# Performance work log

Hardware: AMD Instinct MI355X
Metric: run time of the kernel (lower is better)

The kernel has to match this reference:

```python
import math
import jax, jax.numpy as jnp
import numpy as np

B, C, N, T = 16, 64, 1024, 12


def setup_inputs() -> dict:
    key = jax.random.key(0)
    ks = jax.random.split(key, 12)
    s = 1.0 / math.sqrt(C)
    inp = {
        "input": jax.random.normal(ks[0], (B, C, N, T), dtype=jnp.float32),
        # 1x1 conv weights stored as [out_c, in_c] (squeeze of [C,C,1,1])
        "qw": jax.random.normal(ks[1], (C, C), dtype=jnp.float32) * s,
        "qb": jnp.zeros((C,), dtype=jnp.float32),
        "vw": jax.random.normal(ks[2], (C, C), dtype=jnp.float32) * s,
        "vb": jnp.zeros((C,), dtype=jnp.float32),
        "cw": jax.random.normal(ks[3], (C, C), dtype=jnp.float32) * s,
        "cb": jnp.zeros((C,), dtype=jnp.float32),
        # memory: xavier_uniform over (C, N)
        "memory": jax.random.uniform(ks[4], (C, N), dtype=jnp.float32,
                                      minval=-1.0, maxval=1.0) * math.sqrt(6.0 / (C + N)),
        # fc: Linear(2,8) -> ReLU -> Linear(8,1); torch Linear weight is [out,in]
        "fc1w": jax.random.normal(ks[5], (8, 2), dtype=jnp.float32) * (1.0 / math.sqrt(2.0)),
        "fc1b": jnp.zeros((8,), dtype=jnp.float32),
        "fc2w": jax.random.normal(ks[6], (1, 8), dtype=jnp.float32) * (1.0 / math.sqrt(8.0)),
        "fc2b": jnp.zeros((1,), dtype=jnp.float32),
    }
    return inp


def _conv1x1(x, w, b):
    # Conv2d(C,C,(1,1)) + ReLU (dropout is identity in eval)
    return jax.nn.relu(jnp.einsum('oc,bcnt->bont', w, x) + b[None, :, None, None])


def reference(input, qw, qb, vw, vb, cw, cb, memory, fc1w, fc1b, fc2w, fc2b):
    query = _conv1x1(input, qw, qb)           # [B,C,N,T]
    value = _conv1x1(input, vw, vb)           # [B,C,N,T]
    c = query.shape[1]
    inv_sqrt_c = 1.0 / math.sqrt(c)

    # dynamic adjacency 1: query x memory
    a1 = jax.nn.softmax(
        jax.nn.relu(jnp.einsum('bcnt,cm->bnm', query, memory) * inv_sqrt_c), axis=-1)
    # dynamic adjacency 2: time-pooled query self-similarity
    qs = query.sum(-1)                        # [B,C,N]
    a2 = jax.nn.softmax(
        jax.nn.relu(jnp.einsum('bcn,bcm->bnm', qs, qs) * inv_sqrt_c), axis=-1)

    adj_f = jnp.stack([a1, a2], axis=-1)      # [B,N,N,2]
    h = jax.nn.relu(adj_f @ fc1w.T + fc1b)    # [B,N,N,8]
    adj_f = jax.nn.softmax((h @ fc2w.T + fc2b)[..., 0], axis=-1)  # [B,N,N]

    # top-k mask (k = 0.8*N), scatter 1s at topk indices
    k = int(adj_f.shape[1] * 0.8)
    _, topk_idx = jax.lax.top_k(adj_f, k)     # [B,N,k]
    bsz, n, _ = adj_f.shape
    bi = jnp.arange(bsz)[:, None, None]
    ni = jnp.arange(n)[None, :, None]
    mask = jnp.zeros_like(adj_f).at[bi, ni, topk_idx].set(1.0)
    adj_f = adj_f * mask

    # aggregation: bmm over flattened (C*T)
    b_, cc, nn_, t = value.shape
    vr = value.transpose(0, 2, 1, 3).reshape(b_, nn_, cc * t)   # [B,N,C*T]
    agg = adj_f @ vr                                            # [B,N,C*T]
    agg = agg.reshape(b_, nn_, cc, t).transpose(0, 2, 1, 3)     # [B,C,N,T]

    return _conv1x1(agg, cw, cb)
```

## Files before the change

### kernel.cpp

```cpp
#include <hip/hip_runtime.h>

using u32 = unsigned int;
using u64 = unsigned long long;
using u16 = unsigned short;

typedef __attribute__((ext_vector_type(8))) short bf16x8;
typedef __attribute__((ext_vector_type(4))) float f32x4;

__device__ __forceinline__ u16 f2bf(float f) {
  u32 u = __float_as_uint(f);
  u += 0x7FFFu + ((u >> 16) & 1u);
  return (u16)(u >> 16);
}

__device__ __forceinline__ float wredMaxF(float v) {
#pragma unroll
  for (int o = 32; o > 0; o >>= 1) v = fmaxf(v, __shfl_xor(v, o, 64));
  return v;
}
__device__ __forceinline__ double wredSumD(double v) {
#pragma unroll
  for (int o = 32; o > 0; o >>= 1) v += __shfl_xor(v, o, 64);
  return v;
}

__device__ __forceinline__ float fexpf64(double x) {
  const double INVLN2 = 1.4426950408889634074;
  const double NLN2HI = -6.93147180369123816490e-01;
  const double NLN2LO = -1.90821492927058770002e-10;
  double kd = rint(x * INVLN2);
  double r = fma(kd, NLN2HI, x);
  r = fma(kd, NLN2LO, r);
  double p = 2.08767569878680990e-09;
  p = fma(p, r, 2.50521083854417188e-08);
  p = fma(p, r, 2.75573192239858907e-07);
  p = fma(p, r, 2.75573192239858925e-06);
  p = fma(p, r, 2.48015873015873016e-05);
  p = fma(p, r, 1.98412698412698413e-04);
  p = fma(p, r, 1.38888888888888889e-03);
  p = fma(p, r, 8.33333333333333333e-03);
  p = fma(p, r, 4.16666666666666667e-02);
  p = fma(p, r, 1.66666666666666667e-01);
  p = fma(p, r, 5.0e-01);
  p = fma(p, r, 1.0);
  p = fma(p, r, 1.0);
  int k = (int)kd;
  if (k < -1022) k = -1022;
  double s = __hiloint2double((1023 + k) << 20, 0);
  return (float)(p * s);
}

__global__ __launch_bounds__(512) void k_conv_q(
    const float* __restrict__ x, const float* __restrict__ qw, const float* __restrict__ qb,
    double* __restrict__ qs64, float* __restrict__ qs32T)
{
  __shared__ __align__(16) double Xs64[8 * 384];
  __shared__ float wqT[64 * 65];
  __shared__ float qbL[64];
  const int tid = threadIdx.x;
  const int b = blockIdx.y;
  const int n0 = blockIdx.x * 8;

#pragma unroll
  for (int j = 0; j < 8; ++j) {
    int idx = tid + 512 * j;
    int o = idx >> 6, c = idx & 63;
    wqT[c * 65 + o] = qw[idx];
  }
  if (tid < 64) qbL[tid] = qb[tid];

  const int co = tid & 63;
  const int r = tid >> 6;
  double q0[12];
#pragma unroll
  for (int t = 0; t < 12; ++t) q0[t] = 0.0;

  for (int p = 0; p < 2; ++p) {
    __syncthreads();
#pragma unroll
    for (int j = 0; j < 3; ++j) {
      int d2 = tid + 512 * j;
      int d = d2 * 2;
      int rr = d / 384;
      int rem = d - rr * 384;
      int cl = rem / 12;
      int t = rem - cl * 12;
      float2 f = *(const float2*)&x[(((size_t)(b * 64 + p * 32 + cl)) * 1024 + n0 + rr) * 12 + t];
      double2 dv;
      dv.x = (double)f.x;
      dv.y = (double)f.y;
      *(double2*)&Xs64[d] = dv;
    }
    __syncthreads();

    const double* xrow = &Xs64[r * 384];
#pragma unroll 2
    for (int cl = 0; cl < 32; ++cl) {
      double wd = (double)wqT[(p * 32 + cl) * 65 + co];
      double xd[12];
#pragma unroll
      for (int k = 0; k < 6; ++k)
        *(double2*)&xd[2 * k] = *(const double2*)&xrow[cl * 12 + 2 * k];
#pragma unroll
      for (int t = 0; t < 12; ++t) q0[t] = fma(wd, xd[t], q0[t]);
    }
  }

  const float qbv = qbL[co];
  double sA = 0.0;
#pragma unroll
  for (int t = 0; t < 12; ++t) {
    float qa = fmaxf((float)q0[t] + qbv, 0.f);
    sA += (double)qa;
  }
  qs64[((size_t)(b * 1024 + n0 + r)) * 64 + co] = sA;
  qs32T[((size_t)(b * 64 + co)) * 1024 + n0 + r] = (float)sA;
}

__global__ __launch_bounds__(256) void k_conv_v(
    const float* __restrict__ x, const float* __restrict__ vw, const float* __restrict__ vb,
    u16* __restrict__ vr)
{
  __shared__ float Xs[8 * 768];
  __shared__ float wvT[64 * 64];
  const int tid = threadIdx.x;
  const int b = blockIdx.y;
  const int n0 = blockIdx.x * 8;

#pragma unroll
  for (int j = 0; j < 4; ++j) {
    int lin = (tid + 256 * j) * 4;
    int c = lin >> 6, o0 = lin & 63;
    float4 wv4;
    wv4.x = vw[(o0 + 0) * 64 + c];
    wv4.y = vw[(o0 + 1) * 64 + c];
    wv4.z = vw[(o0 + 2) * 64 + c];
    wv4.w = vw[(o0 + 3) * 64 + c];
    *(float4*)&wvT[lin] = wv4;
  }
#pragma unroll
  for (int j = 0; j < 6; ++j) {
    int q = tid + 256 * j;
    int pr = q / 3, s = q - pr * 3;
    int c = pr >> 3, nl = pr & 7;
    *(float4*)&Xs[nl * 768 + c * 12 + s * 4] =
        *(const float4*)&x[(((size_t)(b * 64 + c)) * 1024 + n0 + nl) * 12 + s * 4];
  }
  __syncthreads();

  const int co = tid & 63;
  const int nlA = tid >> 6;
  const int nlB = nlA + 4;
  float v0[12], v1[12];
#pragma unroll
  for (int t = 0; t < 12; ++t) { v0[t] = 0.f; v1[t] = 0.f; }

  for (int c = 0; c < 64; ++c) {
    float wvv = wvT[c * 64 + co];
    float xA[12], xB[12];
    *(float4*)&xA[0] = *(float4*)&Xs[nlA * 768 + c * 12 + 0];
    *(float4*)&xA[4] = *(float4*)&Xs[nlA * 768 + c * 12 + 4];
    *(float4*)&xA[8] = *(float4*)&Xs[nlA * 768 + c * 12 + 8];
    *(float4*)&xB[0] = *(float4*)&Xs[nlB * 768 + c * 12 + 0];
    *(float4*)&xB[4] = *(float4*)&Xs[nlB * 768 + c * 12 + 4];
    *(float4*)&xB[8] = *(float4*)&Xs[nlB * 768 + c * 12 + 8];
#pragma unroll
    for (int t = 0; t < 12; ++t) {
      v0[t] += wvv * xA[t];
      v1[t] += wvv * xB[t];
    }
  }

  const float vbv = vb[co];
  size_t vb0 = ((size_t)(b * 1024 + n0 + nlA)) * 768 + co * 12;
  size_t vb1 = ((size_t)(b * 1024 + n0 + nlB)) * 768 + co * 12;
#pragma unroll
  for (int i = 0; i < 6; ++i) {
    u32 p0 = (u32)f2bf(fmaxf(v0[2 * i] + vbv, 0.f)) | ((u32)f2bf(fmaxf(v0[2 * i + 1] + vbv, 0.f)) << 16);
    *(u32*)&vr[vb0 + 2 * i] = p0;
    u32 p1 = (u32)f2bf(fmaxf(v1[2 * i] + vbv, 0.f)) | ((u32)f2bf(fmaxf(v1[2 * i + 1] + vbv, 0.f)) << 16);
    *(u32*)&vr[vb1 + 2 * i] = p1;
  }
}

__global__ __launch_bounds__(256) void k_transpose_vr(const u16* __restrict__ vr, u16* __restrict__ vrT)
{
  __shared__ u16 Tt[64 * 72];
  const int tid = threadIdx.x;
  const int b = blockIdx.z;
  const int ct0 = blockIdx.x * 64;
  const int m0 = blockIdx.y * 64;
#pragma unroll
  for (int j = 0; j < 2; ++j) {
    int idx = tid + 256 * j;
    int r = idx >> 3, s = idx & 7;
    u16 tmp[8];
    *(uint4*)tmp = *(const uint4*)&vr[((size_t)(b * 1024 + m0 + r)) * 768 + ct0 + s * 8];
#pragma unroll
    for (int jj = 0; jj < 8; ++jj) Tt[(s * 8 + jj) * 72 + r] = tmp[jj];
  }
  __syncthreads();
#pragma unroll
  for (int j = 0; j < 2; ++j) {
    int idx = tid + 256 * j;
    int r2 = idx >> 3, s2 = idx & 7;
    *(uint4*)&vrT[((size_t)(b * 768 + ct0 + r2)) * 1024 + m0 + s2 * 8] =
        *(const uint4*)&Tt[r2 * 72 + s2 * 8];
  }
}

__global__ __launch_bounds__(256) void k_score(
    const double* __restrict__ qs64, const float* __restrict__ qs32T, const float* __restrict__ mem,
    float* __restrict__ S1, float* __restrict__ S2, int b0)
{
  __shared__ __align__(16) double As64[128 * 17];
  __shared__ __align__(16) double Bm64[16 * 80];
  __shared__ __align__(16) double Bq64[16 * 80];
  const int tid = threadIdx.x;
  const int g = blockIdx.z;
  const int b = b0 + g;
  const int m0 = blockIdx.x * 64;
  const int n0 = blockIdx.y * 128;

  const int mgi  = tid & 7;
  const int ngrp = tid >> 3;

  double acc1[4][8], acc2[4][8];
#pragma unroll
  for (int i = 0; i < 4; ++i)
#pragma unroll
    for (int k = 0; k < 8; ++k) { acc1[i][k] = 0.0; acc2[i][k] = 0.0; }

  for (int ph = 0; ph < 4; ++ph) {
    const int cb = ph * 16;
    __syncthreads();
#pragma unroll
    for (int j = 0; j < 8; ++j) {
      int idx = tid + 256 * j;
      int nl = idx >> 4, c = idx & 15;
      As64[nl * 17 + c] = qs64[((size_t)(b * 1024 + n0 + nl)) * 64 + cb + c];
    }
#pragma unroll
    for (int j = 0; j < 4; ++j) {
      int idx = tid + 256 * j;
      int c = idx >> 6, mm = idx & 63;
      float fm = mem[(size_t)(cb + c) * 1024 + m0 + mm];
      float fq = qs32T[((size_t)(b * 64 + cb + c)) * 1024 + m0 + mm];
      int off = c * 80 + (mm >> 3) * 10 + (mm & 7);
      Bm64[off] = (double)fm;
      Bq64[off] = (double)fq;
    }
    __syncthreads();

    for (int c = 0; c < 16; ++c) {
      double a[4], af[4];
#pragma unroll
      for (int i = 0; i < 4; ++i) {
        a[i] = As64[(ngrp * 4 + i) * 17 + c];
        af[i] = (double)(float)a[i];
      }
      const double* pm = &Bm64[c * 80 + mgi * 10];
      const double* pq = &Bq64[c * 80 + mgi * 10];
#pragma unroll
      for (int kh = 0; kh < 2; ++kh) {
        double bm[4], bq[4];
#pragma unroll
        for (int k = 0; k < 2; ++k) {
          *(double2*)&bm[2 * k] = *(const double2*)&pm[4 * kh + 2 * k];
          *(double2*)&bq[2 * k] = *(const double2*)&pq[4 * kh + 2 * k];
        }
#pragma unroll
        for (int k = 0; k < 4; ++k) {
#pragma unroll
          for (int i = 0; i < 4; ++i) {
            acc1[i][4 * kh + k] = fma(a[i], bm[k], acc1[i][4 * kh + k]);
            acc2[i][4 * kh + k] = fma(af[i], bq[k], acc2[i][4 * kh + k]);
          }
        }
      }
    }
  }
#pragma unroll
  for (int ni = 0; ni < 4; ++ni) {
    size_t off = ((size_t)g * 1024 + n0 + ngrp * 4 + ni) * 1024 + m0 + mgi * 8;
    float o1[8], o2[8];
#pragma unroll
    for (int k = 0; k < 8; ++k) {
      o1[k] = fmaxf((float)(0.125 * acc1[ni][k]), 0.f);
      o2[k] = fmaxf((float)(0.125 * acc2[ni][k]), 0.f);
    }
    *(float4*)&S1[off + 0] = *(float4*)&o1[0];
    *(float4*)&S1[off + 4] = *(float4*)&o1[4];
    *(float4*)&S2[off + 0] = *(float4*)&o2[0];
    *(float4*)&S2[off + 4] = *(float4*)&o2[4];
  }
}

__global__ __launch_bounds__(256) void k_row(
    const float* __restrict__ S1, const float* __restrict__ S2,
    const float* __restrict__ fc1w, const float* __restrict__ fc1b,
    const float* __restrict__ fc2w, const float* __restrict__ fc2b,
    u16* __restrict__ adj, int b0)
{
  const int tid = threadIdx.x;
  const int wv = tid >> 6;
  const int lane = tid & 63;
  const int n = blockIdx.x * 4 + wv;
  const int g = blockIdx.y;

  float w10[8], w11[8], b1s[8], w2s[8];
#pragma unroll
  for (int h = 0; h < 8; ++h) {
    w10[h] = fc1w[2 * h];
    w11[h] = fc1w[2 * h + 1];
    b1s[h] = fc1b[h];
    w2s[h] = fc2w[h];
  }
  const float b2s = fc2b[0];

  const float* r1 = S1 + ((size_t)g * 1024 + n) * 1024;
  const float* r2 = S2 + ((size_t)g * 1024 + n) * 1024;
  const int e0 = lane * 16;
  float s1v[16], s2v[16];
#pragma unroll
  for (int k = 0; k < 4; ++k) {
    *(float4*)&s1v[4 * k] = *(const float4*)&r1[e0 + 4 * k];
    *(float4*)&s2v[4 * k] = *(const float4*)&r2[e0 + 4 * k];
  }

  float lm1 = s1v[0], lm2 = s2v[0];
#pragma unroll
  for (int j = 1; j < 16; ++j) { lm1 = fmaxf(lm1, s1v[j]); lm2 = fmaxf(lm2, s2v[j]); }
  const float m1 = wredMaxF(lm1);
  const float m2 = wredMaxF(lm2);

  float e1[16], e2[16];
  double ls1 = 0.0, ls2 = 0.0;
#pragma unroll
  for (int j = 0; j < 16; ++j) {
    e1[j] = fexpf64((double)(s1v[j] - m1));
    ls1 += (double)e1[j];
    e2[j] = fexpf64((double)(s2v[j] - m2));
    ls2 += (double)e2[j];
  }
  const float Z1f = (float)wredSumD(ls1);
  const float Z2f = (float)wredSumD(ls2);

  float zv[16];
#pragma unroll
  for (int j = 0; j < 16; ++j) {
    float a1 = e1[j] / Z1f;
    float a2 = e2[j] / Z2f;
    float acc = 0.f;
#pragma unroll
    for (int h = 0; h < 8; ++h) {
      float hp = __fmaf_rn(a2, w11[h], __fmaf_rn(a1, w10[h], 0.0f));
      hp = hp + b1s[h];
      float hr = fmaxf(hp, 0.f);
      acc = __fmaf_rn(hr, w2s[h], acc);
    }
    zv[j] = acc + b2s;
  }

  float lmz = zv[0];
#pragma unroll
  for (int j = 1; j < 16; ++j) lmz = fmaxf(lmz, zv[j]);
  const float mz = wredMaxF(lmz);
  float ez[16];
  double lsz = 0.0;
#pragma unroll
  for (int j = 0; j < 16; ++j) {
    ez[j] = fexpf64((double)(zv[j] - mz));
    lsz += (double)ez[j];
  }
  const float Zzf = (float)wredSumD(lsz);

  u32 kreg[16];
#pragma unroll
  for (int j = 0; j < 16; ++j) kreg[j] = __float_as_uint(ez[j] / Zzf);

  u32 vkey = 0u;
  for (int bit = 30; bit >= 0; --bit) {
    u32 cand = vkey | (1u << bit);
    u32 cnt = 0u;
#pragma unroll
    for (int j = 0; j < 16; ++j)
      cnt += (u32)__popcll(__ballot(kreg[j] >= cand));
    if (cnt >= 819u) vkey = cand;
  }
  u32 cntGT = 0u;
#pragma unroll
  for (int j = 0; j < 16; ++j)
    cntGT += (u32)__popcll(__ballot(kreg[j] > vkey));
  const u32 need_eq = 819u - cntGT;

  int cnt = 0;
#pragma unroll
  for (int j = 0; j < 16; ++j) cnt += (kreg[j] == vkey) ? 1 : 0;
  u32 inc = (u32)cnt;
#pragma unroll
  for (int o = 1; o < 64; o <<= 1) {
    u32 nv = __shfl_up(inc, o, 64);
    if (lane >= o) inc += nv;
  }
  u32 run = inc - (u32)cnt;

  u16 ov[16];
#pragma unroll
  for (int j = 0; j < 16; ++j) {
    u32 kk = kreg[j];
    bool eq = (kk == vkey);
    bool keep = (kk > vkey) || (eq && (run < need_eq));
    if (eq) run += 1u;
    ov[j] = keep ? f2bf(__uint_as_float(kk)) : (u16)0;
  }
  u16* arow = adj + ((size_t)(b0 + g) * 1024 + n) * 1024 + e0;
  *(uint4*)&arow[0] = *(uint4*)&ov[0];
  *(uint4*)&arow[8] = *(uint4*)&ov[8];
}

__global__ __launch_bounds__(256) void k_gemm_agg(
    const u16* __restrict__ adj, const u16* __restrict__ vrT, float* __restrict__ agg)
{
  __shared__ u16 As[128 * 40];
  __shared__ u16 Bs[128 * 40];
  const int tid = threadIdx.x;
  const int b = blockIdx.z;
  const int n0 = blockIdx.y * 128;
  const int ct0 = blockIdx.x * 128;
  const int wid = tid >> 6;
  const int lane = tid & 63;
  const int l16 = lane & 15;
  const int quad = lane >> 4;
  const int wm = (wid >> 1) * 64;
  const int wn = (wid & 1) * 64;

  f32x4 acc[4][4];
#pragma unroll
  for (int i = 0; i < 4; ++i)
#pragma unroll
    for (int j = 0; j < 4; ++j) acc[i][j] = (f32x4)0.f;

  const u16* aG = adj + ((size_t)b * 1024 + n0) * 1024;
  const u16* bG = vrT + ((size_t)b * 768 + ct0) * 1024;

  for (int kt = 0; kt < 32; ++kt) {
    const int k0 = kt * 32;
    __syncthreads();
#pragma unroll
    for (int j = 0; j < 2; ++j) {
      int idx = tid + 256 * j;
      int row = idx >> 2, seg = idx & 3;
      *(uint4*)&As[row * 40 + seg * 8] = *(const uint4*)&aG[(size_t)row * 1024 + k0 + seg * 8];
      *(uint4*)&Bs[row * 40 + seg * 8] = *(const uint4*)&bG[(size_t)row * 1024 + k0 + seg * 8];
    }
    __syncthreads();
    bf16x8 af[4], bfv[4];
#pragma unroll
    for (int i = 0; i < 4; ++i) af[i] = *(bf16x8*)&As[(wm + i * 16 + l16) * 40 + quad * 8];
#pragma unroll
    for (int j = 0; j < 4; ++j) bfv[j] = *(bf16x8*)&Bs[(wn + j * 16 + l16) * 40 + quad * 8];
#pragma unroll
    for (int i = 0; i < 4; ++i)
#pragma unroll
      for (int j = 0; j < 4; ++j)
        acc[i][j] = __builtin_amdgcn_mfma_f32_16x16x32_bf16(af[i], bfv[j], acc[i][j], 0, 0, 0);
  }

#pragma unroll
  for (int i = 0; i < 4; ++i)
#pragma unroll
    for (int j = 0; j < 4; ++j)
#pragma unroll
      for (int r = 0; r < 4; ++r) {
        int row = n0 + wm + i * 16 + quad * 4 + r;
        int col = ct0 + wn + j * 16 + l16;
        agg[((size_t)b * 1024 + row) * 768 + col] = acc[i][j][r];
      }
}

__global__ __launch_bounds__(256) void k_convc(
    const float* __restrict__ agg, const float* __restrict__ cw,
    const float* __restrict__ cb, float* __restrict__ out)
{
  __shared__ float aggL[16 * 388];
  __shared__ float cwT[64 * 68];
  __shared__ float cbL[64];
  const int tid = threadIdx.x;
  const int b = blockIdx.y;
  const int n0 = blockIdx.x * 16;

#pragma unroll
  for (int j = 0; j < 16; ++j) {
    int idx = tid + 256 * j;
    int o = idx >> 6, c = idx & 63;
    cwT[c * 68 + o] = cw[idx];
  }
  if (tid < 64) cbL[tid] = cb[tid];

  const int o0 = (tid & 15) * 4;
  const int nl = tid >> 4;
  float acc[4][12];
#pragma unroll
  for (int oo = 0; oo < 4; ++oo)
#pragma unroll
    for (int t = 0; t < 12; ++t) acc[oo][t] = 0.f;

  for (int ph = 0; ph < 2; ++ph) {
    __syncthreads();
#pragma unroll
    for (int j = 0; j < 6; ++j) {
      int q4 = tid + 256 * j;
      int row = q4 / 96, wi = q4 - row * 96;
      *(float4*)&aggL[row * 388 + wi * 4] =
          *(const float4*)&agg[((size_t)(b * 1024 + n0 + row)) * 768 + ph * 384 + wi * 4];
    }
    __syncthreads();
    for (int cc = 0; cc < 32; ++cc) {
      int c = ph * 32 + cc;
      float4 w4 = *(float4*)&cwT[c * 68 + o0];
      float xr[12];
      *(float4*)&xr[0] = *(float4*)&aggL[nl * 388 + cc * 12 + 0];
      *(float4*)&xr[4] = *(float4*)&aggL[nl * 388 + cc * 12 + 4];
      *(float4*)&xr[8] = *(float4*)&aggL[nl * 388 + cc * 12 + 8];
#pragma unroll
      for (int t = 0; t < 12; ++t) {
        acc[0][t] += w4.x * xr[t];
        acc[1][t] += w4.y * xr[t];
        acc[2][t] += w4.z * xr[t];
        acc[3][t] += w4.w * xr[t];
      }
    }
  }

#pragma unroll
  for (int oo = 0; oo < 4; ++oo) {
    int o = o0 + oo;
    float bias = cbL[o];
    float ovv[12];
#pragma unroll
    for (int t = 0; t < 12; ++t) ovv[t] = fmaxf(acc[oo][t] + bias, 0.f);
    size_t base = ((size_t)(b * 64 + o) * 1024 + n0 + nl) * 12;
    *(float4*)&out[base + 0] = *(float4*)&ovv[0];
    *(float4*)&out[base + 4] = *(float4*)&ovv[4];
    *(float4*)&out[base + 8] = *(float4*)&ovv[8];
  }
}

extern "C" void kernel_launch(void* const* d_in, const int* in_sizes, int n_in,
                              void* d_out, int out_size, void* d_ws, size_t ws_size,
                              hipStream_t stream)
{
  const float* x    = (const float*)d_in[0];
  const float* qw   = (const float*)d_in[1];
  const float* qb   = (const float*)d_in[2];
  const float* vw   = (const float*)d_in[3];
  const float* vb   = (const float*)d_in[4];
  const float* cw   = (const float*)d_in[5];
  const float* cb   = (const float*)d_in[6];
  const float* mem  = (const float*)d_in[7];
  const float* fc1w = (const float*)d_in[8];
  const float* fc1b = (const float*)d_in[9];
  const float* fc2w = (const float*)d_in[10];
  const float* fc2b = (const float*)d_in[11];
  float* out = (float*)d_out;
  char* ws = (char*)d_ws;

  const size_t szQS64  = (size_t)16 * 1024 * 64 * 8;
  const size_t szQS32T = (size_t)16 * 1024 * 64 * 4;
  const size_t szVR    = (size_t)16 * 1024 * 768 * 2;
  const size_t szADJ   = (size_t)16 * 1024 * 1024 * 2;
  const size_t szAGG   = (size_t)16 * 1024 * 768 * 4;
  const size_t szSb    = (size_t)1024 * 1024 * 4;
  const size_t fixed   = szQS64 + szQS32T + 2 * szVR + szADJ + szAGG;

  int G = 16;
  while (G > 1 && (fixed + (size_t)2 * G * szSb) > ws_size) G >>= 1;

  double* qs64  = (double*)(ws);
  float*  qs32T = (float*)(ws + szQS64);
  u16*  vr      = (u16*)(ws + szQS64 + szQS32T);
  u16*  vrT     = (u16*)(ws + szQS64 + szQS32T + szVR);
  u16*  adj     = (u16*)(ws + szQS64 + szQS32T + 2 * szVR);
  float* agg    = (float*)(ws + szQS64 + szQS32T + 2 * szVR + szADJ);
  float* S1     = (float*)(ws + fixed);
  float* S2     = S1 + (size_t)G * 1024 * 1024;

  hipLaunchKernelGGL(k_conv_q, dim3(128, 16), dim3(512), 0, stream, x, qw, qb, qs64, qs32T);
  hipLaunchKernelGGL(k_conv_v, dim3(128, 16), dim3(256), 0, stream, x, vw, vb, vr);
  hipLaunchKernelGGL(k_transpose_vr, dim3(12, 16, 16), dim3(256), 0, stream, vr, vrT);
  for (int b0 = 0; b0 < 16; b0 += G) {
    hipLaunchKernelGGL(k_score, dim3(16, 8, G), dim3(256), 0, stream, qs64, qs32T, mem, S1, S2, b0);
    hipLaunchKernelGGL(k_row, dim3(256, G), dim3(256), 0, stream, S1, S2, fc1w, fc1b, fc2w, fc2b, adj, b0);
  }
  hipLaunchKernelGGL(k_gemm_agg, dim3(6, 8, 16), dim3(256), 0, stream, adj, vrT, agg);
  hipLaunchKernelGGL(k_convc, dim3(64, 16), dim3(256), 0, stream, agg, cw, cb, out);
}
```

Measured before the change: 505.0 us.

## Load GEMM tiles directly into LDS with swizzle; restructure q conv

The aggregation GEMM now stages its A/B tiles with global_load_lds (direct global-to-LDS DMA). It uses an XOR-swizzled unpadded layout in place of padded register-staged copies, which cuts VGPR traffic and bank conflicts. Separately, the q convolution drops its LDS staging of inputs converted to double. Each wavefront now handles one node and reads its x row straight from global memory with wave-uniform addresses, broadcast across lanes. The risks are reliance on the global_load_lds lane-to-address mapping matching the swizzle, and uncoalesced broadcast loads in conv_q.

```diff
diff --git a/kernel.cpp b/kernel.cpp
--- a/kernel.cpp
+++ b/kernel.cpp
@@ -22,6 +22,11 @@
 #pragma unroll
   for (int o = 32; o > 0; o >>= 1) v += __shfl_xor(v, o, 64);
   return v;
+}
+
+__device__ __forceinline__ void gload16(const void* g, void* l) {
+  __builtin_amdgcn_global_load_lds((const __attribute__((address_space(1))) void*)g,
+                                   (__attribute__((address_space(3))) void*)l, 16, 0, 0);
 }
 
 __device__ __forceinline__ float fexpf64(double x) {
@@ -50,71 +55,54 @@
   return (float)(p * s);
 }
 
-__global__ __launch_bounds__(512) void k_conv_q(
+__global__ __launch_bounds__(256) void k_conv_q(
     const float* __restrict__ x, const float* __restrict__ qw, const float* __restrict__ qb,
     double* __restrict__ qs64, float* __restrict__ qs32T)
 {
-  __shared__ __align__(16) double Xs64[8 * 384];
   __shared__ float wqT[64 * 65];
   __shared__ float qbL[64];
   const int tid = threadIdx.x;
   const int b = blockIdx.y;
-  const int n0 = blockIdx.x * 8;
-
-#pragma unroll
-  for (int j = 0; j < 8; ++j) {
-    int idx = tid + 512 * j;
+
+#pragma unroll
+  for (int j = 0; j < 16; ++j) {
+    int idx = tid + 256 * j;
     int o = idx >> 6, c = idx & 63;
     wqT[c * 65 + o] = qw[idx];
   }
   if (tid < 64) qbL[tid] = qb[tid];
-
-  const int co = tid & 63;
-  const int r = tid >> 6;
+  __syncthreads();
+
+  const int lane = tid & 63;
+  const int n = blockIdx.x * 4 + (tid >> 6);
+  const int base = __builtin_amdgcn_readfirstlane((b * 64 * 1024 + n) * 12);
+  const float* __restrict__ xr = x + base;
+
   double q0[12];
 #pragma unroll
   for (int t = 0; t < 12; ++t) q0[t] = 0.0;
 
-  for (int p = 0; p < 2; ++p) {
-    __syncthreads();
-#pragma unroll
-    for (int j = 0; j < 3; ++j) {
-      int d2 = tid + 512 * j;
-      int d = d2 * 2;
-      int rr = d / 384;
-      int rem = d - rr * 384;
-      int cl = rem / 12;
-      int t = rem - cl * 12;
-      float2 f = *(const float2*)&x[(((size_t)(b * 64 + p * 32 + cl)) * 1024 + n0 + rr) * 12 + t];
-      double2 dv;
-      dv.x = (double)f.x;
-      dv.y = (double)f.y;
-      *(double2*)&Xs64[d] = dv;
-    }
-    __syncthreads();
-
-    const double* xrow = &Xs64[r * 384];
-#pragma unroll 2
-    for (int cl = 0; cl < 32; ++cl) {
-      double wd = (double)wqT[(p * 32 + cl) * 65 + co];
-      double xd[12];
-#pragma unroll
-      for (int k = 0; k < 6; ++k)
-        *(double2*)&xd[2 * k] = *(const double2*)&xrow[cl * 12 + 2 * k];
-#pragma unroll
-      for (int t = 0; t < 12; ++t) q0[t] = fma(wd, xd[t], q0[t]);
-    }
-  }
-
-  const float qbv = qbL[co];
+#pragma unroll 4
+  for (int c = 0; c < 64; ++c) {
+    const float* p = xr + c * 12288;
+    float xf[12];
+    *(float4*)&xf[0] = *(const float4*)&p[0];
+    *(float4*)&xf[4] = *(const float4*)&p[4];
+    *(float4*)&xf[8] = *(const float4*)&p[8];
+    double wd = (double)wqT[c * 65 + lane];
+#pragma unroll
+    for (int t = 0; t < 12; ++t) q0[t] = fma(wd, (double)xf[t], q0[t]);
+  }
+
+  const float qbv = qbL[lane];
   double sA = 0.0;
 #pragma unroll
   for (int t = 0; t < 12; ++t) {
     float qa = fmaxf((float)q0[t] + qbv, 0.f);
     sA += (double)qa;
   }
-  qs64[((size_t)(b * 1024 + n0 + r)) * 64 + co] = sA;
-  qs32T[((size_t)(b * 64 + co)) * 1024 + n0 + r] = (float)sA;
+  qs64[((size_t)(b * 1024 + n)) * 64 + lane] = sA;
+  qs32T[((size_t)(b * 64 + lane)) * 1024 + n] = (float)sA;
 }
 
 __global__ __launch_bounds__(256) void k_conv_v(
@@ -422,8 +410,8 @@
 __global__ __launch_bounds__(256) void k_gemm_agg(
     const u16* __restrict__ adj, const u16* __restrict__ vrT, float* __restrict__ agg)
 {
-  __shared__ u16 As[128 * 40];
-  __shared__ u16 Bs[128 * 40];
+  __shared__ __align__(16) u16 As[128 * 32];
+  __shared__ __align__(16) u16 Bs[128 * 32];
   const int tid = threadIdx.x;
   const int b = blockIdx.z;
   const int n0 = blockIdx.y * 128;
@@ -435,6 +423,10 @@
   const int wm = (wid >> 1) * 64;
   const int wn = (wid & 1) * 64;
 
+  const int lr = lane >> 2;
+  const int ss8 = (((lane & 3) ^ ((lane >> 3) & 3)) * 8);
+  const int segR = ((quad ^ ((l16 >> 1) & 3)) * 8);
+
   f32x4 acc[4][4];
 #pragma unroll
   for (int i = 0; i < 4; ++i)
@@ -449,17 +441,16 @@
     __syncthreads();
 #pragma unroll
     for (int j = 0; j < 2; ++j) {
-      int idx = tid + 256 * j;
-      int row = idx >> 2, seg = idx & 3;
-      *(uint4*)&As[row * 40 + seg * 8] = *(const uint4*)&aG[(size_t)row * 1024 + k0 + seg * 8];
-      *(uint4*)&Bs[row * 40 + seg * 8] = *(const uint4*)&bG[(size_t)row * 1024 + k0 + seg * 8];
+      int row = wid * 32 + j * 16 + lr;
+      gload16(aG + (size_t)row * 1024 + k0 + ss8, &As[(wid * 32 + j * 16) * 32]);
+      gload16(bG + (size_t)row * 1024 + k0 + ss8, &Bs[(wid * 32 + j * 16) * 32]);
     }
     __syncthreads();
     bf16x8 af[4], bfv[4];
 #pragma unroll
-    for (int i = 0; i < 4; ++i) af[i] = *(bf16x8*)&As[(wm + i * 16 + l16) * 40 + quad * 8];
-#pragma unroll
-    for (int j = 0; j < 4; ++j) bfv[j] = *(bf16x8*)&Bs[(wn + j * 16 + l16) * 40 + quad * 8];
+    for (int i = 0; i < 4; ++i) af[i] = *(bf16x8*)&As[(wm + i * 16 + l16) * 32 + segR];
+#pragma unroll
+    for (int j = 0; j < 4; ++j) bfv[j] = *(bf16x8*)&Bs[(wn + j * 16 + l16) * 32 + segR];
 #pragma unroll
     for (int i = 0; i < 4; ++i)
 #pragma unroll
@@ -586,7 +577,7 @@
   float* S1     = (float*)(ws + fixed);
   float* S2     = S1 + (size_t)G * 1024 * 1024;
 
-  hipLaunchKernelGGL(k_conv_q, dim3(128, 16), dim3(512), 0, stream, x, qw, qb, qs64, qs32T);
+  hipLaunchKernelGGL(k_conv_q, dim3(256, 16), dim3(256), 0, stream, x, qw, qb, qs64, qs32T);
   hipLaunchKernelGGL(k_conv_v, dim3(128, 16), dim3(256), 0, stream, x, vw, vb, vr);
   hipLaunchKernelGGL(k_transpose_vr, dim3(12, 16, 16), dim3(256), 0, stream, vr, vrT);
   for (int b0 = 0; b0 < 16; b0 += G) {
```

New measurement: 544.5 us. 1.08x slower.

## Fuse query and value 1x1 convs into one kernel sharing input tile

Applied to the files above, without the earlier changes.

Merges the separate query (fp64 accumulate) and value (fp32) 1x1 conv kernels into one kernel that loads each input tile into shared memory once and computes both outputs. Weight transposes move to a tiny pre-kernel writing to workspace, and weights are read from global/L1 instead of LDS. This removes one full read of the input tensor and a kernel launch. In exchange it adds a launch, uses more blocks with smaller tiles, and mixes fp64 and fp32 FMAs per thread, which raises register pressure.

```diff
diff --git a/kernel.cpp b/kernel.cpp
--- a/kernel.cpp
+++ b/kernel.cpp
@@ -50,136 +50,78 @@
   return (float)(p * s);
 }
 
-__global__ __launch_bounds__(512) void k_conv_q(
-    const float* __restrict__ x, const float* __restrict__ qw, const float* __restrict__ qb,
-    double* __restrict__ qs64, float* __restrict__ qs32T)
-{
-  __shared__ __align__(16) double Xs64[8 * 384];
-  __shared__ float wqT[64 * 65];
-  __shared__ float qbL[64];
+__global__ __launch_bounds__(1024) void k_wT(
+    const float* __restrict__ qw, const float* __restrict__ vw,
+    float* __restrict__ wqTg, float* __restrict__ wvTg)
+{
+  int idx = blockIdx.x * 1024 + threadIdx.x;
+  int o = idx >> 6, c = idx & 63;
+  wqTg[c * 64 + o] = qw[idx];
+  wvTg[c * 64 + o] = vw[idx];
+}
+
+__global__ __launch_bounds__(256, 8) void k_conv_qv(
+    const float* __restrict__ x, const float* __restrict__ wqTg, const float* __restrict__ qb,
+    const float* __restrict__ wvTg, const float* __restrict__ vb,
+    double* __restrict__ qs64, float* __restrict__ qs32T, u16* __restrict__ vr)
+{
+  __shared__ float Xs[4 * 768];
   const int tid = threadIdx.x;
   const int b = blockIdx.y;
-  const int n0 = blockIdx.x * 8;
-
-#pragma unroll
-  for (int j = 0; j < 8; ++j) {
-    int idx = tid + 512 * j;
-    int o = idx >> 6, c = idx & 63;
-    wqT[c * 65 + o] = qw[idx];
-  }
-  if (tid < 64) qbL[tid] = qb[tid];
+  const int n0 = blockIdx.x * 4;
+
+#pragma unroll
+  for (int j = 0; j < 3; ++j) {
+    int q = tid + 256 * j;
+    int pr = q / 3, s = q - pr * 3;
+    int c = pr >> 2, nl = pr & 3;
+    *(float4*)&Xs[nl * 768 + c * 12 + s * 4] =
+        *(const float4*)&x[(((size_t)(b * 64 + c)) * 1024 + n0 + nl) * 12 + s * 4];
+  }
+  __syncthreads();
 
   const int co = tid & 63;
-  const int r = tid >> 6;
+  const int nl = tid >> 6;
+  const float* xrow = &Xs[nl * 768];
+
   double q0[12];
-#pragma unroll
-  for (int t = 0; t < 12; ++t) q0[t] = 0.0;
-
-  for (int p = 0; p < 2; ++p) {
-    __syncthreads();
-#pragma unroll
-    for (int j = 0; j < 3; ++j) {
-      int d2 = tid + 512 * j;
-      int d = d2 * 2;
-      int rr = d / 384;
-      int rem = d - rr * 384;
-      int cl = rem / 12;
-      int t = rem - cl * 12;
-      float2 f = *(const float2*)&x[(((size_t)(b * 64 + p * 32 + cl)) * 1024 + n0 + rr) * 12 + t];
-      double2 dv;
-      dv.x = (double)f.x;
-      dv.y = (double)f.y;
-      *(double2*)&Xs64[d] = dv;
-    }
-    __syncthreads();
-
-    const double* xrow = &Xs64[r * 384];
+  float v0[12];
+#pragma unroll
+  for (int t = 0; t < 12; ++t) { q0[t] = 0.0; v0[t] = 0.f; }
+
 #pragma unroll 2
-    for (int cl = 0; cl < 32; ++cl) {
-      double wd = (double)wqT[(p * 32 + cl) * 65 + co];
-      double xd[12];
-#pragma unroll
-      for (int k = 0; k < 6; ++k)
-        *(double2*)&xd[2 * k] = *(const double2*)&xrow[cl * 12 + 2 * k];
-#pragma unroll
-      for (int t = 0; t < 12; ++t) q0[t] = fma(wd, xd[t], q0[t]);
-    }
-  }
-
-  const float qbv = qbL[co];
+  for (int c = 0; c < 64; ++c) {
+    float wq = wqTg[c * 64 + co];
+    float wv = wvTg[c * 64 + co];
+    float xf[12];
+    *(float4*)&xf[0] = *(const float4*)&xrow[c * 12 + 0];
+    *(float4*)&xf[4] = *(const float4*)&xrow[c * 12 + 4];
+    *(float4*)&xf[8] = *(const float4*)&xrow[c * 12 + 8];
+    double wqd = (double)wq;
+#pragma unroll
+    for (int t = 0; t < 12; ++t) {
+      q0[t] = fma(wqd, (double)xf[t], q0[t]);
+      v0[t] += wv * xf[t];
+    }
+  }
+
+  const float qbv = qb[co];
+  const float vbv = vb[co];
   double sA = 0.0;
 #pragma unroll
   for (int t = 0; t < 12; ++t) {
     float qa = fmaxf((float)q0[t] + qbv, 0.f);
     sA += (double)qa;
   }
-  qs64[((size_t)(b * 1024 + n0 + r)) * 64 + co] = sA;
-  qs32T[((size_t)(b * 64 + co)) * 1024 + n0 + r] = (float)sA;
-}
-
-__global__ __launch_bounds__(256) void k_conv_v(
-    const float* __restrict__ x, const float* __restrict__ vw, const float* __restrict__ vb,
-    u16* __restrict__ vr)
-{
-  __shared__ float Xs[8 * 768];
-  __shared__ float wvT[64 * 64];
-  const int tid = threadIdx.x;
-  const int b = blockIdx.y;
-  const int n0 = blockIdx.x * 8;
-
-#pragma unroll
-  for (int j = 0; j < 4; ++j) {
-    int lin = (tid + 256 * j) * 4;
-    int c = lin >> 6, o0 = lin & 63;
-    float4 wv4;
-    wv4.x = vw[(o0 + 0) * 64 + c];
-    wv4.y = vw[(o0 + 1) * 64 + c];
-    wv4.z = vw[(o0 + 2) * 64 + c];
-    wv4.w = vw[(o0 + 3) * 64 + c];
-    *(float4*)&wvT[lin] = wv4;
-  }
-#pragma unroll
-  for (int j = 0; j < 6; ++j) {
-    int q = tid + 256 * j;
-    int pr = q / 3, s = q - pr * 3;
-    int c = pr >> 3, nl = pr & 7;
-    *(float4*)&Xs[nl * 768 + c * 12 + s * 4] =
-        *(const float4*)&x[(((size_t)(b * 64 + c)) * 1024 + n0 + nl) * 12 + s * 4];
-  }
-  __syncthreads();
-
-  const int co = tid & 63;
-  const int nlA = tid >> 6;
-  const int nlB = nlA + 4;
-  float v0[12], v1[12];
-#pragma unroll
-  for (int t = 0; t < 12; ++t) { v0[t] = 0.f; v1[t] = 0.f; }
-
-  for (int c = 0; c < 64; ++c) {
-    float wvv = wvT[c * 64 + co];
-    float xA[12], xB[12];
-    *(float4*)&xA[0] = *(float4*)&Xs[nlA * 768 + c * 12 + 0];
-    *(float4*)&xA[4] = *(float4*)&Xs[nlA * 768 + c * 12 + 4];
-    *(float4*)&xA[8] = *(float4*)&Xs[nlA * 768 + c * 12 + 8];
-    *(float4*)&xB[0] = *(float4*)&Xs[nlB * 768 + c * 12 + 0];
-    *(float4*)&xB[4] = *(float4*)&Xs[nlB * 768 + c * 12 + 4];
-    *(float4*)&xB[8] = *(float4*)&Xs[nlB * 768 + c * 12 + 8];
-#pragma unroll
-    for (int t = 0; t < 12; ++t) {
-      v0[t] += wvv * xA[t];
-      v1[t] += wvv * xB[t];
-    }
-  }
-
-  const float vbv = vb[co];
-  size_t vb0 = ((size_t)(b * 1024 + n0 + nlA)) * 768 + co * 12;
-  size_t vb1 = ((size_t)(b * 1024 + n0 + nlB)) * 768 + co * 12;
+  const int n = n0 + nl;
+  qs64[((size_t)(b * 1024 + n)) * 64 + co] = sA;
+  qs32T[((size_t)(b * 64 + co)) * 1024 + n] = (float)sA;
+
+  size_t vb0 = ((size_t)(b * 1024 + n)) * 768 + co * 12;
 #pragma unroll
   for (int i = 0; i < 6; ++i) {
     u32 p0 = (u32)f2bf(fmaxf(v0[2 * i] + vbv, 0.f)) | ((u32)f2bf(fmaxf(v0[2 * i + 1] + vbv, 0.f)) << 16);
     *(u32*)&vr[vb0 + 2 * i] = p0;
-    u32 p1 = (u32)f2bf(fmaxf(v1[2 * i] + vbv, 0.f)) | ((u32)f2bf(fmaxf(v1[2 * i + 1] + vbv, 0.f)) << 16);
-    *(u32*)&vr[vb1 + 2 * i] = p1;
   }
 }
 
@@ -571,8 +513,9 @@
   const size_t szVR    = (size_t)16 * 1024 * 768 * 2;
   const size_t szADJ   = (size_t)16 * 1024 * 1024 * 2;
   const size_t szAGG   = (size_t)16 * 1024 * 768 * 4;
+  const size_t szWT    = (size_t)2 * 64 * 64 * 4;
   const size_t szSb    = (size_t)1024 * 1024 * 4;
-  const size_t fixed   = szQS64 + szQS32T + 2 * szVR + szADJ + szAGG;
+  const size_t fixed   = szQS64 + szQS32T + 2 * szVR + szADJ + szAGG + szWT;
 
   int G = 16;
   while (G > 1 && (fixed + (size_t)2 * G * szSb) > ws_size) G >>= 1;
@@ -583,11 +526,13 @@
   u16*  vrT     = (u16*)(ws + szQS64 + szQS32T + szVR);
   u16*  adj     = (u16*)(ws + szQS64 + szQS32T + 2 * szVR);
   float* agg    = (float*)(ws + szQS64 + szQS32T + 2 * szVR + szADJ);
+  float* wqTg   = (float*)(ws + szQS64 + szQS32T + 2 * szVR + szADJ + szAGG);
+  float* wvTg   = wqTg + 64 * 64;
   float* S1     = (float*)(ws + fixed);
   float* S2     = S1 + (size_t)G * 1024 * 1024;
 
-  hipLaunchKernelGGL(k_conv_q, dim3(128, 16), dim3(512), 0, stream, x, qw, qb, qs64, qs32T);
-  hipLaunchKernelGGL(k_conv_v, dim3(128, 16), dim3(256), 0, stream, x, vw, vb, vr);
+  hipLaunchKernelGGL(k_wT, dim3(4), dim3(1024), 0, stream, qw, vw, wqTg, wvTg);
+  hipLaunchKernelGGL(k_conv_qv, dim3(256, 16), dim3(256), 0, stream, x, wqTg, qb, wvTg, vb, qs64, qs32T, vr);
   hipLaunchKernelGGL(k_transpose_vr, dim3(12, 16, 16), dim3(256), 0, stream, vr, vrT);
   for (int b0 = 0; b0 < 16; b0 += G) {
     hipLaunchKernelGGL(k_score, dim3(16, 8, G), dim3(256), 0, stream, qs64, qs32T, mem, S1, S2, b0);
```

Result: slower. 530.8 us (+5.1%).
